# Performance work log

Measured on AMD Instinct MI355X. Metric: run time of the kernel, lower is better.

The kernel has to match this reference:

```python
import jax, jax.numpy as jnp
import numpy as np

TAU_PLUS = 0.02
TAU_MINUS = 0.02
TAU_X = 0.101
A_TRIPLET = 0.0065
HOMEOSTATIC_RATE = 0.1
DT = 0.001
SPIKE_P = 0.05  # spike probability used to binarize inputs


def setup_inputs() -> dict:
    key = jax.random.key(0)
    k1, k2, k3 = jax.random.split(key, 3)
    B, P, Q, T = 16, 2048, 2048, 256
    pre_spikes = (jax.random.uniform(k1, (B, P, T)) < SPIKE_P).astype(jnp.float32)
    post_spikes = (jax.random.uniform(k2, (B, Q, T)) < SPIKE_P).astype(jnp.float32)
    weights = jax.random.normal(k3, (P, Q), dtype=jnp.float32) * 0.1
    meta_A_plus = jnp.float32(0.01)
    meta_A_minus = jnp.float32(0.012)
    return {"pre_spikes": pre_spikes, "post_spikes": post_spikes,
            "weights": weights, "meta_A_plus": meta_A_plus,
            "meta_A_minus": meta_A_minus}


def _traces(spikes_tbn, decay):
    """Trace value used at step t: x_t = decay * (x_{t-1} + s_{t-1}), x_0 = 0."""
    def step(carry, s):
        x = decay * carry          # decayed trace, used for this step's update
        return x + s, x            # spike added AFTER the update, per original
    init = jnp.zeros(spikes_tbn.shape[1:], spikes_tbn.dtype)
    _, xs = jax.lax.scan(step, init, spikes_tbn)
    return xs  # [T, B, N]


def reference(pre_spikes, post_spikes, weights, meta_A_plus, meta_A_minus):
    B, P, T = pre_spikes.shape
    exp_plus = jnp.exp(jnp.float32(-DT / TAU_PLUS))
    exp_minus = jnp.exp(jnp.float32(-DT / TAU_MINUS))
    exp_x = jnp.exp(jnp.float32(-DT / TAU_X))

    pre_t = jnp.transpose(pre_spikes, (2, 0, 1))    # [T, B, P]
    post_t = jnp.transpose(post_spikes, (2, 0, 1))  # [T, B, Q]

    x_pre = _traces(pre_t, exp_plus)     # [T, B, P]
    x_post = _traces(post_t, exp_minus)  # [T, B, Q]
    x_trip = _traces(post_t, exp_x)      # [T, B, Q]

    # Per-step outer products summed over time == one big contraction over (t, b).
    ltp = jnp.einsum('tbp,tbq->pq', x_pre, post_t) * meta_A_plus
    triplet = jnp.einsum('tbp,tbq->pq', x_pre, post_t * x_trip) * A_TRIPLET
    ltd = jnp.einsum('tbp,tbq->pq', pre_t, x_post) * meta_A_minus
    weight_updates = ltp + triplet - ltd

    # Homeostatic scaling (fresh module: activity history holds only this sample)
    current_activity = (pre_spikes.sum() + post_spikes.sum()) / (B * T)
    scaling_factor = jnp.sqrt(HOMEOSTATIC_RATE / (current_activity + 1e-6))

    updated_weights = weights + weight_updates * scaling_factor
    return jnp.clip(updated_weights, -2.0, 2.0)
```

## Files before the change

### kernel.cpp

```cpp
#include <hip/hip_runtime.h>

constexpr int TB = 16;
constexpr int NP = 2048;
constexpr int NQ = 2048;
constexpr int TT = 256;
constexpr int KH = TB * TT;
constexpr int KT = 2 * KH;

typedef unsigned short ushort_t;
typedef __attribute__((ext_vector_type(8))) __bf16 bf16x8;
typedef __attribute__((ext_vector_type(4))) float f32x4;

__device__ __forceinline__ unsigned bf1(float f) {
    unsigned u = __builtin_bit_cast(unsigned, f);
    return (u + 0x7FFFu + ((u >> 16) & 1u)) >> 16;
}
__device__ __forceinline__ unsigned pack2(float lo, float hi) {
    return bf1(lo) | (bf1(hi) << 16);
}
__device__ __forceinline__ unsigned spk2(float a, float b) {
    return ((a != 0.f) ? 0x3F80u : 0u) | ((b != 0.f) ? 0x3F800000u : 0u);
}

constexpr float DF1 = 0.95122942450071400910f;
constexpr float DF2 = DF1 * DF1;
constexpr float DF4 = DF2 * DF2;
constexpr float DF8 = DF4 * DF4;
constexpr float DF16 = DF8 * DF8;
constexpr float DF32 = DF16 * DF16;
constexpr float DF64 = DF32 * DF32;

constexpr float DX1 = 0.99014786386058731819f;
constexpr float DX2 = DX1 * DX1;
constexpr float DX4 = DX2 * DX2;
constexpr float DX8 = DX4 * DX4;
constexpr float DX16 = DX8 * DX8;
constexpr float DX32 = DX16 * DX16;
constexpr float DX64 = DX32 * DX32;

template <int K>
__device__ __forceinline__ float seg_step(float b, float pw, int sl) {
    float t = __shfl_up(b, K, 64);
    return (sl >= K) ? fmaf(pw, t, b) : b;
}
__device__ __forceinline__ float scan16(float c, float p1, float p2, float p4,
                                        float p8, int sl) {
    c = seg_step<1>(c, p1, sl);
    c = seg_step<2>(c, p2, sl);
    c = seg_step<4>(c, p4, sl);
    c = seg_step<8>(c, p8, sl);
    return c;
}

__device__ __forceinline__ float fold4(float4 u, float d) {
    float C = d * u.x;
    C = d * (C + u.y); C = d * (C + u.z); C = d * (C + u.w);
    return C;
}
__device__ __forceinline__ float4 expand4(float x, float4 u, float d) {
    float4 t;
    t.x = x; x = d * (x + u.x);
    t.y = x; x = d * (x + u.y);
    t.z = x; x = d * (x + u.z);
    t.w = x;
    return t;
}

__global__ __launch_bounds__(256) void stage_traces(
    const float* __restrict__ pre, const float* __restrict__ post,
    const float* __restrict__ mApP, const float* __restrict__ mAmP,
    ushort_t* __restrict__ Ab, ushort_t* __restrict__ Bb,
    float* __restrict__ partials)
{
    const int tid  = threadIdx.x;
    const int lane = tid & 63;
    const int wv   = tid >> 6;
    const int sl   = lane & 15;
    const int rowg = blockIdx.x * 16 + wv * 4 + (lane >> 4);
    const bool isPre = rowg < TB * NP;
    const int m = isPre ? rowg : rowg - TB * NP;
    const int b = m >> 11;
    const int r = m & 2047;

    const float4* srcRow = (const float4*)((isPre ? pre : post) + (size_t)m * TT);
    const float4 u0 = srcRow[sl];
    const float4 u1 = srcRow[16 + sl];
    const float4 u2 = srcRow[32 + sl];
    const float4 u3 = srcRow[48 + sl];

    float cnt = ((u0.x + u0.y) + (u0.z + u0.w)) + ((u1.x + u1.y) + (u1.z + u1.w))
              + ((u2.x + u2.y) + (u2.z + u2.w)) + ((u3.x + u3.y) + (u3.z + u3.w));

    const int hi = lane | 15;

    float bf0 = scan16(fold4(u0, DF1), DF4, DF8, DF16, DF32, sl);
    float bf1_ = scan16(fold4(u1, DF1), DF4, DF8, DF16, DF32, sl);
    float bf2 = scan16(fold4(u2, DF1), DF4, DF8, DF16, DF32, sl);
    float bf3 = scan16(fold4(u3, DF1), DF4, DF8, DF16, DF32, sl);
    const float Tf0 = __shfl(bf0, hi, 64);
    const float Tf1 = __shfl(bf1_, hi, 64);
    const float Tf2 = __shfl(bf2, hi, 64);
    const float Xf1 = Tf0;
    const float Xf2 = fmaf(DF64, Xf1, Tf1);
    const float Xf3 = fmaf(DF64, Xf2, Tf2);
    float ef0 = __shfl_up(bf0, 1, 64);
    float ef1 = __shfl_up(bf1_, 1, 64);
    float ef2 = __shfl_up(bf2, 1, 64);
    float ef3 = __shfl_up(bf3, 1, 64);
    if (sl == 0) { ef0 = 0.f; ef1 = 0.f; ef2 = 0.f; ef3 = 0.f; }
    float pf = 1.f;
    if (sl & 1) pf *= DF4;
    if (sl & 2) pf *= DF8;
    if (sl & 4) pf *= DF16;
    if (sl & 8) pf *= DF32;
    const float4 t0 = expand4(ef0,                 u0, DF1);
    const float4 t1 = expand4(fmaf(pf, Xf1, ef1),  u1, DF1);
    const float4 t2 = expand4(fmaf(pf, Xf2, ef2),  u2, DF1);
    const float4 t3 = expand4(fmaf(pf, Xf3, ef3),  u3, DF1);

    ushort_t* oA = (isPre ? Ab : Bb) + (size_t)r * KT + b * TT + 4 * sl;

    if (isPre) {
        *(uint2*)(oA)            = uint2{pack2(t0.x, t0.y), pack2(t0.z, t0.w)};
        *(uint2*)(oA + 64)       = uint2{pack2(t1.x, t1.y), pack2(t1.z, t1.w)};
        *(uint2*)(oA + 128)      = uint2{pack2(t2.x, t2.y), pack2(t2.z, t2.w)};
        *(uint2*)(oA + 192)      = uint2{pack2(t3.x, t3.y), pack2(t3.z, t3.w)};
        *(uint2*)(oA + KH)       = uint2{spk2(u0.x, u0.y), spk2(u0.z, u0.w)};
        *(uint2*)(oA + KH + 64)  = uint2{spk2(u1.x, u1.y), spk2(u1.z, u1.w)};
        *(uint2*)(oA + KH + 128) = uint2{spk2(u2.x, u2.y), spk2(u2.z, u2.w)};
        *(uint2*)(oA + KH + 192) = uint2{spk2(u3.x, u3.y), spk2(u3.z, u3.w)};
    } else {
        float bx0 = scan16(fold4(u0, DX1), DX4, DX8, DX16, DX32, sl);
        float bx1 = scan16(fold4(u1, DX1), DX4, DX8, DX16, DX32, sl);
        float bx2 = scan16(fold4(u2, DX1), DX4, DX8, DX16, DX32, sl);
        float bx3 = scan16(fold4(u3, DX1), DX4, DX8, DX16, DX32, sl);
        const float Tx0 = __shfl(bx0, hi, 64);
        const float Tx1 = __shfl(bx1, hi, 64);
        const float Tx2 = __shfl(bx2, hi, 64);
        const float Xx1 = Tx0;
        const float Xx2 = fmaf(DX64, Xx1, Tx1);
        const float Xx3 = fmaf(DX64, Xx2, Tx2);
        float ex0 = __shfl_up(bx0, 1, 64);
        float ex1 = __shfl_up(bx1, 1, 64);
        float ex2 = __shfl_up(bx2, 1, 64);
        float ex3 = __shfl_up(bx3, 1, 64);
        if (sl == 0) { ex0 = 0.f; ex1 = 0.f; ex2 = 0.f; ex3 = 0.f; }
        float px = 1.f;
        if (sl & 1) px *= DX4;
        if (sl & 2) px *= DX8;
        if (sl & 4) px *= DX16;
        if (sl & 8) px *= DX32;
        const float4 w0 = expand4(ex0,                u0, DX1);
        const float4 w1 = expand4(fmaf(px, Xx1, ex1), u1, DX1);
        const float4 w2 = expand4(fmaf(px, Xx2, ex2), u2, DX1);
        const float4 w3 = expand4(fmaf(px, Xx3, ex3), u3, DX1);

        const float Ap = *mApP;
        const float Am = *mAmP;
        auto av2 = [&](float sa, float ta, float sb, float tb) -> unsigned {
            unsigned lo = (sa != 0.f) ? bf1(fmaf(0.0065f, ta, Ap)) : 0u;
            unsigned hi2 = (sb != 0.f) ? bf1(fmaf(0.0065f, tb, Ap)) : 0u;
            return lo | (hi2 << 16);
        };
        *(uint2*)(oA)       = uint2{av2(u0.x, w0.x, u0.y, w0.y), av2(u0.z, w0.z, u0.w, w0.w)};
        *(uint2*)(oA + 64)  = uint2{av2(u1.x, w1.x, u1.y, w1.y), av2(u1.z, w1.z, u1.w, w1.w)};
        *(uint2*)(oA + 128) = uint2{av2(u2.x, w2.x, u2.y, w2.y), av2(u2.z, w2.z, u2.w, w2.w)};
        *(uint2*)(oA + 192) = uint2{av2(u3.x, w3.x, u3.y, w3.y), av2(u3.z, w3.z, u3.w, w3.w)};
        *(uint2*)(oA + KH)       = uint2{pack2(-Am * t0.x, -Am * t0.y), pack2(-Am * t0.z, -Am * t0.w)};
        *(uint2*)(oA + KH + 64)  = uint2{pack2(-Am * t1.x, -Am * t1.y), pack2(-Am * t1.z, -Am * t1.w)};
        *(uint2*)(oA + KH + 128) = uint2{pack2(-Am * t2.x, -Am * t2.y), pack2(-Am * t2.z, -Am * t2.w)};
        *(uint2*)(oA + KH + 192) = uint2{pack2(-Am * t3.x, -Am * t3.y), pack2(-Am * t3.z, -Am * t3.w)};
    }

    #pragma unroll
    for (int off = 32; off > 0; off >>= 1)
        cnt += __shfl_down(cnt, off, 64);
    __shared__ float wsum[4];
    if (lane == 0) wsum[wv] = cnt;
    __syncthreads();
    if (tid == 0)
        partials[blockIdx.x] = (wsum[0] + wsum[1]) + (wsum[2] + wsum[3]);
}

__device__ __forceinline__ void async16(const ushort_t* g, ushort_t* l) {
    __builtin_amdgcn_global_load_lds(
        (const __attribute__((address_space(1))) unsigned int*)g,
        (__attribute__((address_space(3))) unsigned int*)l,
        16, 0, 0);
}

__global__ __launch_bounds__(256, 2) void gemm_split(
    const ushort_t* __restrict__ Ab, const ushort_t* __restrict__ Bb,
    const float* __restrict__ sp, float* __restrict__ scaleBuf,
    float* __restrict__ P0, float* __restrict__ P1)
{
    __shared__ ushort_t As[2][128 * 64];
    __shared__ ushort_t Bs[2][128 * 64];
    __shared__ float red[4];

    const int tid  = threadIdx.x;
    const int lane = tid & 63;
    const int wv   = tid >> 6;
    const int wr   = wv >> 1;
    const int wc   = wv & 1;
    const int quad = lane >> 4;
    const int m16  = lane & 15;

    if (blockIdx.x == 0) {
        float v = 0.f;
        #pragma unroll
        for (int i = 0; i < 16; ++i) v += sp[tid + i * 256];
        #pragma unroll
        for (int off = 32; off > 0; off >>= 1)
            v += __shfl_down(v, off, 64);
        if (lane == 0) red[wv] = v;
        __syncthreads();
        if (tid == 0) {
            float s = (red[0] + red[1]) + (red[2] + red[3]);
            scaleBuf[0] = sqrtf(0.1f / (s * (1.0f / 4096.0f) + 1e-6f));
        }
    }

    const int id  = blockIdx.x;
    const int xcd = id & 7;
    const int j5  = id >> 3;
    const int z   = j5 & 1;
    const int t   = j5 >> 1;
    const int pt  = ((xcd >> 1) << 2) + (t >> 3);
    const int qt  = ((xcd & 1) << 3) + (t & 7);

    const int p0 = pt * 128;
    const int q0 = qt * 128;
    const int kbase = z * (KT / 2);
    const int ldsbase = wv * 512;

    const ushort_t* gaP[4];
    const ushort_t* gbP[4];
    #pragma unroll
    for (int rr = 0; rr < 4; ++rr) {
        const int c   = rr * 256 + tid;
        const int row = c >> 3;
        const int kk8 = (c & 7) ^ (row & 7);
        gaP[rr] = Ab + (size_t)(p0 + row) * KT + kbase + kk8 * 8;
        gbP[rr] = Bb + (size_t)(q0 + row) * KT + kbase + kk8 * 8;
    }

    f32x4 acc[4][4] = {};

    auto stageF = [&](int buf) {
        #pragma unroll
        for (int rr = 0; rr < 4; ++rr) {
            async16(gaP[rr], &As[buf][rr * 2048 + ldsbase]);
            async16(gbP[rr], &Bs[buf][rr * 2048 + ldsbase]);
            gaP[rr] += 64;
            gbP[rr] += 64;
        }
    };
    auto computeF = [&](int buf) {
        #pragma unroll
        for (int ks = 0; ks < 2; ++ks) {
            bf16x8 af[4], bf[4];
            #pragma unroll
            for (int i = 0; i < 4; ++i) {
                const int row  = wr * 64 + i * 16 + m16;
                const int slot = (ks * 4 + quad) ^ (row & 7);
                af[i] = *(const bf16x8*)&As[buf][row * 64 + slot * 8];
            }
            #pragma unroll
            for (int jj = 0; jj < 4; ++jj) {
                const int row  = wc * 64 + jj * 16 + m16;
                const int slot = (ks * 4 + quad) ^ (row & 7);
                bf[jj] = *(const bf16x8*)&Bs[buf][row * 64 + slot * 8];
            }
            #pragma unroll
            for (int i = 0; i < 4; ++i)
                #pragma unroll
                for (int jj = 0; jj < 4; ++jj)
                    acc[i][jj] = __builtin_amdgcn_mfma_f32_16x16x32_bf16(
                        af[i], bf[jj], acc[i][jj], 0, 0, 0);
        }
    };

    constexpr int NIT = (KT / 2) / 64;
    stageF(0);
    for (int kt2 = 0; kt2 < NIT / 2; ++kt2) {
        __syncthreads();
        stageF(1);
        computeF(0);
        __syncthreads();
        if (kt2 + 1 < NIT / 2)
            stageF(0);
        computeF(1);
    }

    float* P = z ? P1 : P0;
    #pragma unroll
    for (int i = 0; i < 4; ++i) {
        const int prow = p0 + wr * 64 + i * 16 + quad * 4;
        #pragma unroll
        for (int jj = 0; jj < 4; ++jj) {
            const int qcol = q0 + wc * 64 + jj * 16 + m16;
            #pragma unroll
            for (int r2 = 0; r2 < 4; ++r2)
                P[(size_t)(prow + r2) * NQ + qcol] = acc[i][jj][r2];
        }
    }
}

__global__ __launch_bounds__(256) void merge_out(
    const float* __restrict__ W, const float* __restrict__ P1,
    const float* __restrict__ scaleBuf, float* __restrict__ Out)
{
    const float scale = scaleBuf[0];
    const size_t i4 = (size_t)blockIdx.x * 256 + threadIdx.x;
    float4 w = ((const float4*)W)[i4];
    float4 a = ((const float4*)Out)[i4];
    float4 c = ((const float4*)P1)[i4];
    float4 o;
    o.x = fminf(fmaxf(fmaf(scale, a.x + c.x, w.x), -2.f), 2.f);
    o.y = fminf(fmaxf(fmaf(scale, a.y + c.y, w.y), -2.f), 2.f);
    o.z = fminf(fmaxf(fmaf(scale, a.z + c.z, w.z), -2.f), 2.f);
    o.w = fminf(fmaxf(fmaf(scale, a.w + c.w, w.w), -2.f), 2.f);
    ((float4*)Out)[i4] = o;
}

extern "C" void kernel_launch(void* const* d_in, const int* in_sizes, int n_in,
                              void* d_out, int out_size, void* d_ws, size_t ws_size,
                              hipStream_t stream) {
    const float* pre  = (const float*)d_in[0];
    const float* post = (const float*)d_in[1];
    const float* W    = (const float*)d_in[2];
    const float* mAp  = (const float*)d_in[3];
    const float* mAm  = (const float*)d_in[4];
    float* out = (float*)d_out;

    char* ws = (char*)d_ws;
    float* partials = (float*)ws;
    float* scaleBuf = (float*)(ws + 16384);
    ushort_t* Ab = (ushort_t*)(ws + 32768);
    ushort_t* Bb = (ushort_t*)(ws + 32768 + (size_t)NP * KT * 2);
    float* P1    = (float*)(ws + 32768 + 2 * (size_t)NP * KT * 2);

    stage_traces<<<dim3((TB * NP + TB * NQ) / 16), dim3(256), 0, stream>>>(
        pre, post, mAp, mAm, Ab, Bb, partials);

    gemm_split<<<dim3(512), dim3(256), 0, stream>>>(
        Ab, Bb, partials, scaleBuf, out, P1);

    merge_out<<<dim3(NP * NQ / 1024), dim3(256), 0, stream>>>(
        W, P1, scaleBuf, out);
}
```

Before: 199.6 us.

## Fuse split-K reduction and epilogue into GEMM via intra-block LDS reduction

Replaces the two-block split-K GEMM plus separate merge kernel with one 512-thread block per output tile. Two 256-thread groups each cover half of K, then reduce their accumulators through LDS, and the epilogue applies scale, weights and the clip directly. The homeostatic scale is now computed redundantly in every block. This removes the partial-sum write and re-read through global memory and one kernel launch, at the cost of halving the block count to 256 and using 128KB of dynamic LDS. It also switches the bf16 packing to the hardware pack-convert instruction when that builtin is available.

```diff
diff --git a/kernel.cpp b/kernel.cpp
--- a/kernel.cpp
+++ b/kernel.cpp
@@ -9,17 +9,32 @@
 
 typedef unsigned short ushort_t;
 typedef __attribute__((ext_vector_type(8))) __bf16 bf16x8;
+typedef __attribute__((ext_vector_type(2))) __bf16 bf16x2_t;
 typedef __attribute__((ext_vector_type(4))) float f32x4;
+
+#if defined(__has_builtin)
+#if __has_builtin(__builtin_amdgcn_cvt_pk_bf16_f32)
+#define HW_PK 1
+#endif
+#endif
 
 __device__ __forceinline__ unsigned bf1(float f) {
     unsigned u = __builtin_bit_cast(unsigned, f);
     return (u + 0x7FFFu + ((u >> 16) & 1u)) >> 16;
 }
 __device__ __forceinline__ unsigned pack2(float lo, float hi) {
+#ifdef HW_PK
+    bf16x2_t p = __builtin_amdgcn_cvt_pk_bf16_f32(lo, hi);
+    return __builtin_bit_cast(unsigned, p);
+#else
     return bf1(lo) | (bf1(hi) << 16);
+#endif
 }
 __device__ __forceinline__ unsigned spk2(float a, float b) {
     return ((a != 0.f) ? 0x3F80u : 0u) | ((b != 0.f) ? 0x3F800000u : 0u);
+}
+__device__ __forceinline__ float gate(float s, float x) {
+    return (s != 0.f) ? x : 0.f;
 }
 
 constexpr float DF1 = 0.95122942450071400910f;
@@ -51,7 +66,6 @@
     c = seg_step<8>(c, p8, sl);
     return c;
 }
-
 __device__ __forceinline__ float fold4(float4 u, float d) {
     float C = d * u.x;
     C = d * (C + u.y); C = d * (C + u.z); C = d * (C + u.w);
@@ -157,15 +171,18 @@
 
         const float Ap = *mApP;
         const float Am = *mAmP;
-        auto av2 = [&](float sa, float ta, float sb, float tb) -> unsigned {
-            unsigned lo = (sa != 0.f) ? bf1(fmaf(0.0065f, ta, Ap)) : 0u;
-            unsigned hi2 = (sb != 0.f) ? bf1(fmaf(0.0065f, tb, Ap)) : 0u;
-            return lo | (hi2 << 16);
-        };
-        *(uint2*)(oA)       = uint2{av2(u0.x, w0.x, u0.y, w0.y), av2(u0.z, w0.z, u0.w, w0.w)};
-        *(uint2*)(oA + 64)  = uint2{av2(u1.x, w1.x, u1.y, w1.y), av2(u1.z, w1.z, u1.w, w1.w)};
-        *(uint2*)(oA + 128) = uint2{av2(u2.x, w2.x, u2.y, w2.y), av2(u2.z, w2.z, u2.w, w2.w)};
-        *(uint2*)(oA + 192) = uint2{av2(u3.x, w3.x, u3.y, w3.y), av2(u3.z, w3.z, u3.w, w3.w)};
+        *(uint2*)(oA) = uint2{
+            pack2(gate(u0.x, fmaf(0.0065f, w0.x, Ap)), gate(u0.y, fmaf(0.0065f, w0.y, Ap))),
+            pack2(gate(u0.z, fmaf(0.0065f, w0.z, Ap)), gate(u0.w, fmaf(0.0065f, w0.w, Ap)))};
+        *(uint2*)(oA + 64) = uint2{
+            pack2(gate(u1.x, fmaf(0.0065f, w1.x, Ap)), gate(u1.y, fmaf(0.0065f, w1.y, Ap))),
+            pack2(gate(u1.z, fmaf(0.0065f, w1.z, Ap)), gate(u1.w, fmaf(0.0065f, w1.w, Ap)))};
+        *(uint2*)(oA + 128) = uint2{
+            pack2(gate(u2.x, fmaf(0.0065f, w2.x, Ap)), gate(u2.y, fmaf(0.0065f, w2.y, Ap))),
+            pack2(gate(u2.z, fmaf(0.0065f, w2.z, Ap)), gate(u2.w, fmaf(0.0065f, w2.w, Ap)))};
+        *(uint2*)(oA + 192) = uint2{
+            pack2(gate(u3.x, fmaf(0.0065f, w3.x, Ap)), gate(u3.y, fmaf(0.0065f, w3.y, Ap))),
+            pack2(gate(u3.z, fmaf(0.0065f, w3.z, Ap)), gate(u3.w, fmaf(0.0065f, w3.w, Ap)))};
         *(uint2*)(oA + KH)       = uint2{pack2(-Am * t0.x, -Am * t0.y), pack2(-Am * t0.z, -Am * t0.w)};
         *(uint2*)(oA + KH + 64)  = uint2{pack2(-Am * t1.x, -Am * t1.y), pack2(-Am * t1.z, -Am * t1.w)};
         *(uint2*)(oA + KH + 128) = uint2{pack2(-Am * t2.x, -Am * t2.y), pack2(-Am * t2.z, -Am * t2.w)};
@@ -189,56 +206,56 @@
         16, 0, 0);
 }
 
-__global__ __launch_bounds__(256, 2) void gemm_split(
+__global__ __launch_bounds__(512, 1) void gemm_fused(
     const ushort_t* __restrict__ Ab, const ushort_t* __restrict__ Bb,
-    const float* __restrict__ sp, float* __restrict__ scaleBuf,
-    float* __restrict__ P0, float* __restrict__ P1)
+    const float* __restrict__ sp, const float* __restrict__ W,
+    float* __restrict__ Out)
 {
-    __shared__ ushort_t As[2][128 * 64];
-    __shared__ ushort_t Bs[2][128 * 64];
-    __shared__ float red[4];
+    extern __shared__ ushort_t smem[];
+    __shared__ float red[8];
 
     const int tid  = threadIdx.x;
     const int lane = tid & 63;
     const int wv   = tid >> 6;
-    const int wr   = wv >> 1;
-    const int wc   = wv & 1;
+    const int g    = wv >> 2;
+    const int w4   = wv & 3;
+    const int wr   = w4 >> 1;
+    const int wc   = w4 & 1;
     const int quad = lane >> 4;
     const int m16  = lane & 15;
-
-    if (blockIdx.x == 0) {
+    const int tg   = tid & 255;
+
+    {
         float v = 0.f;
         #pragma unroll
-        for (int i = 0; i < 16; ++i) v += sp[tid + i * 256];
+        for (int i = 0; i < 8; ++i) v += sp[tid + i * 512];
         #pragma unroll
         for (int off = 32; off > 0; off >>= 1)
             v += __shfl_down(v, off, 64);
         if (lane == 0) red[wv] = v;
-        __syncthreads();
-        if (tid == 0) {
-            float s = (red[0] + red[1]) + (red[2] + red[3]);
-            scaleBuf[0] = sqrtf(0.1f / (s * (1.0f / 4096.0f) + 1e-6f));
-        }
-    }
+    }
+    __syncthreads();
+    const float ssum = ((red[0] + red[1]) + (red[2] + red[3]))
+                     + ((red[4] + red[5]) + (red[6] + red[7]));
+    const float scale = sqrtf(0.1f / (ssum * (1.0f / 4096.0f) + 1e-6f));
 
     const int id  = blockIdx.x;
     const int xcd = id & 7;
-    const int j5  = id >> 3;
-    const int z   = j5 & 1;
-    const int t   = j5 >> 1;
+    const int t   = id >> 3;
     const int pt  = ((xcd >> 1) << 2) + (t >> 3);
     const int qt  = ((xcd & 1) << 3) + (t & 7);
 
     const int p0 = pt * 128;
     const int q0 = qt * 128;
-    const int kbase = z * (KT / 2);
-    const int ldsbase = wv * 512;
+    const int kbase = g * KH;
+
+    ushort_t* Lg = smem + g * 32768;
 
     const ushort_t* gaP[4];
     const ushort_t* gbP[4];
     #pragma unroll
     for (int rr = 0; rr < 4; ++rr) {
-        const int c   = rr * 256 + tid;
+        const int c   = rr * 256 + tg;
         const int row = c >> 3;
         const int kk8 = (c & 7) ^ (row & 7);
         gaP[rr] = Ab + (size_t)(p0 + row) * KT + kbase + kk8 * 8;
@@ -248,40 +265,44 @@
     f32x4 acc[4][4] = {};
 
     auto stageF = [&](int buf) {
+        ushort_t* dstA = Lg + buf * 8192 + w4 * 512;
+        ushort_t* dstB = Lg + 16384 + buf * 8192 + w4 * 512;
         #pragma unroll
         for (int rr = 0; rr < 4; ++rr) {
-            async16(gaP[rr], &As[buf][rr * 2048 + ldsbase]);
-            async16(gbP[rr], &Bs[buf][rr * 2048 + ldsbase]);
+            async16(gaP[rr], dstA + rr * 2048);
+            async16(gbP[rr], dstB + rr * 2048);
             gaP[rr] += 64;
             gbP[rr] += 64;
         }
     };
     auto computeF = [&](int buf) {
+        const ushort_t* A = Lg + buf * 8192;
+        const ushort_t* B = Lg + 16384 + buf * 8192;
         #pragma unroll
         for (int ks = 0; ks < 2; ++ks) {
-            bf16x8 af[4], bf[4];
+            bf16x8 af[4], bfr[4];
             #pragma unroll
             for (int i = 0; i < 4; ++i) {
                 const int row  = wr * 64 + i * 16 + m16;
                 const int slot = (ks * 4 + quad) ^ (row & 7);
-                af[i] = *(const bf16x8*)&As[buf][row * 64 + slot * 8];
+                af[i] = *(const bf16x8*)&A[row * 64 + slot * 8];
             }
             #pragma unroll
             for (int jj = 0; jj < 4; ++jj) {
                 const int row  = wc * 64 + jj * 16 + m16;
                 const int slot = (ks * 4 + quad) ^ (row & 7);
-                bf[jj] = *(const bf16x8*)&Bs[buf][row * 64 + slot * 8];
+                bfr[jj] = *(const bf16x8*)&B[row * 64 + slot * 8];
             }
             #pragma unroll
             for (int i = 0; i < 4; ++i)
                 #pragma unroll
                 for (int jj = 0; jj < 4; ++jj)
                     acc[i][jj] = __builtin_amdgcn_mfma_f32_16x16x32_bf16(
-                        af[i], bf[jj], acc[i][jj], 0, 0, 0);
+                        af[i], bfr[jj], acc[i][jj], 0, 0, 0);
         }
     };
 
-    constexpr int NIT = (KT / 2) / 64;
+    constexpr int NIT = KH / 64;
     stageF(0);
     for (int kt2 = 0; kt2 < NIT / 2; ++kt2) {
         __syncthreads();
@@ -293,35 +314,41 @@
         computeF(1);
     }
 
-    float* P = z ? P1 : P0;
-    #pragma unroll
-    for (int i = 0; i < 4; ++i) {
-        const int prow = p0 + wr * 64 + i * 16 + quad * 4;
-        #pragma unroll
-        for (int jj = 0; jj < 4; ++jj) {
-            const int qcol = q0 + wc * 64 + jj * 16 + m16;
-            #pragma unroll
-            for (int r2 = 0; r2 < 4; ++r2)
-                P[(size_t)(prow + r2) * NQ + qcol] = acc[i][jj][r2];
+    __syncthreads();
+    float* accL = (float*)smem;
+    if (g == 1) {
+        #pragma unroll
+        for (int i = 0; i < 4; ++i) {
+            const int rowb = wr * 64 + i * 16 + quad * 4;
+            #pragma unroll
+            for (int jj = 0; jj < 4; ++jj) {
+                const int col = wc * 64 + jj * 16 + m16;
+                #pragma unroll
+                for (int r2 = 0; r2 < 4; ++r2)
+                    accL[(rowb + r2) * 132 + col] = acc[i][jj][r2];
+            }
         }
     }
-}
-
-__global__ __launch_bounds__(256) void merge_out(
-    const float* __restrict__ W, const float* __restrict__ P1,
-    const float* __restrict__ scaleBuf, float* __restrict__ Out)
-{
-    const float scale = scaleBuf[0];
-    const size_t i4 = (size_t)blockIdx.x * 256 + threadIdx.x;
-    float4 w = ((const float4*)W)[i4];
-    float4 a = ((const float4*)Out)[i4];
-    float4 c = ((const float4*)P1)[i4];
-    float4 o;
-    o.x = fminf(fmaxf(fmaf(scale, a.x + c.x, w.x), -2.f), 2.f);
-    o.y = fminf(fmaxf(fmaf(scale, a.y + c.y, w.y), -2.f), 2.f);
-    o.z = fminf(fmaxf(fmaf(scale, a.z + c.z, w.z), -2.f), 2.f);
-    o.w = fminf(fmaxf(fmaf(scale, a.w + c.w, w.w), -2.f), 2.f);
-    ((float4*)Out)[i4] = o;
+    __syncthreads();
+    if (g == 0) {
+        #pragma unroll
+        for (int i = 0; i < 4; ++i) {
+            const int rowb = wr * 64 + i * 16 + quad * 4;
+            #pragma unroll
+            for (int jj = 0; jj < 4; ++jj) {
+                const int col = wc * 64 + jj * 16 + m16;
+                #pragma unroll
+                for (int r2 = 0; r2 < 4; ++r2) {
+                    const size_t idx = (size_t)(p0 + rowb + r2) * NQ + (q0 + col);
+                    float o = fmaf(scale,
+                                   acc[i][jj][r2] + accL[(rowb + r2) * 132 + col],
+                                   W[idx]);
+                    o = fminf(fmaxf(o, -2.f), 2.f);
+                    Out[idx] = o;
+                }
+            }
+        }
+    }
 }
 
 extern "C" void kernel_launch(void* const* d_in, const int* in_sizes, int n_in,
@@ -336,17 +363,15 @@
 
     char* ws = (char*)d_ws;
     float* partials = (float*)ws;
-    float* scaleBuf = (float*)(ws + 16384);
     ushort_t* Ab = (ushort_t*)(ws + 32768);
     ushort_t* Bb = (ushort_t*)(ws + 32768 + (size_t)NP * KT * 2);
-    float* P1    = (float*)(ws + 32768 + 2 * (size_t)NP * KT * 2);
 
     stage_traces<<<dim3((TB * NP + TB * NQ) / 16), dim3(256), 0, stream>>>(
         pre, post, mAp, mAm, Ab, Bb, partials);
 
-    gemm_split<<<dim3(512), dim3(256), 0, stream>>>(
-        Ab, Bb, partials, scaleBuf, out, P1);
-
-    merge_out<<<dim3(NP * NQ / 1024), dim3(256), 0, stream>>>(
-        W, P1, scaleBuf, out);
-}
+    hipFuncSetAttribute((const void*)gemm_fused,
+                        hipFuncAttributeMaxDynamicSharedMemorySize, 131072);
+
+    gemm_fused<<<dim3(256), dim3(512), 131072, stream>>>(
+        Ab, Bb, partials, W, out);
+}
```

New measurement: 202.4 us. About the same (+1.4%).
